# Performance work log

Hardware: AMD Instinct MI355X
Metric: run time of the kernel (lower is better)

The kernel has to match this reference:

```python
import jax, jax.numpy as jnp
import numpy as np

N = 100000   # nodes
E = 1600000  # edges (avg degree 16)
D = 64       # feature dim
H = 256      # MLP hidden
EPS = 0.0    # init_eps, learn_eps=False


def setup_inputs() -> dict:
    key = jax.random.key(0)
    k = jax.random.split(key, 5)
    feat = jax.random.normal(k[0], (N, D), dtype=jnp.float32)
    W1 = jax.random.normal(k[1], (D, H), dtype=jnp.float32) / np.sqrt(D)
    b1 = jnp.zeros((H,), dtype=jnp.float32)
    W2 = jax.random.normal(k[2], (H, D), dtype=jnp.float32) / np.sqrt(H)
    b2 = jnp.zeros((D,), dtype=jnp.float32)
    src = jax.random.randint(k[3], (E,), 0, N, dtype=jnp.int32)
    dst = jax.random.randint(k[4], (E,), 0, N, dtype=jnp.int32)
    return {"feat": feat, "W1": W1, "b1": b1, "W2": W2, "b2": b2,
            "src": src, "dst": dst}


def reference(feat, W1, b1, W2, b2, src, dst):
    # message: m_e = feat[src_e]; reduce: sum over edges into dst
    neigh = jax.ops.segment_sum(feat[src], dst, num_segments=N)  # [N, D]
    # eps-scaled self loop (no edge features => feat_dst unpadded)
    rst = (1.0 + EPS) * feat + neigh
    # apply_func: 2-layer MLP with ReLU
    h = jax.nn.relu(rst @ W1 + b1)
    return h @ W2 + b2
```

## Files before the change

kernel.cpp:

```cpp
#include <hip/hip_runtime.h>

#define D 64
#define H 256
#define SRC_MASK ((1u << 23) - 1)

#define NBF 512
#define NPBF 256
#define CAPF 4096
#define PJ 8
#define PROUNDS 2

#define NB2 512
#define NPB2 256
#define CAP2 6144
#define PEPT 16

typedef __bf16 bf16x8 __attribute__((ext_vector_type(8)));
typedef float f32x16 __attribute__((ext_vector_type(16)));
typedef unsigned int uint4v __attribute__((ext_vector_type(4)));

__device__ inline unsigned pack_bf16x2(float a, float b) {
    unsigned short ua = __builtin_bit_cast(unsigned short, (__bf16)a);
    unsigned short ub = __builtin_bit_cast(unsigned short, (__bf16)b);
    return (unsigned)ua | ((unsigned)ub << 16);
}

__device__ inline void lane32_swap(unsigned x, unsigned y, unsigned& o0, unsigned& o1) {
#if __has_builtin(__builtin_amdgcn_permlane32_swap)
    typedef unsigned int uint2v __attribute__((ext_vector_type(2)));
    uint2v r = __builtin_amdgcn_permlane32_swap(x, y, false, false);
    o0 = r.x; o1 = r.y;
#else
    unsigned xs = __shfl_xor((int)x, 32, 64);
    unsigned ys = __shfl_xor((int)y, 32, 64);
    bool hi = (threadIdx.x & 32) != 0;
    o0 = hi ? ys : x;
    o1 = hi ? y : xs;
#endif
}

__device__ inline bf16x8 weight_frag(const float* __restrict__ W1,
                                     const float* __restrict__ W2,
                                     int fid, int lane) {
    int g = lane >> 5, c = lane & 31;
    bf16x8 v;
    if (fid < 32) {
        int ht = fid >> 2, ks = fid & 3;
        const float* col = W1 + (32 * ht + c);
        int k0 = 16 * ks + 8 * g;
#pragma unroll
        for (int j = 0; j < 8; ++j) v[j] = (__bf16)col[(size_t)(k0 + j) * H];
    } else {
        int f = fid - 32;
        int dt = f >> 4, ks = f & 15;
        const float* col = W2 + (32 * dt + c);
        int k0 = 16 * ks + 8 * g;
#pragma unroll
        for (int j = 0; j < 8; ++j) v[j] = (__bf16)col[(size_t)(k0 + j) * D];
    }
    return v;
}

__global__ __launch_bounds__(1024) void fused_front_kernel(
        const float* __restrict__ feat, unsigned short* __restrict__ featb,
        int n8v,
        const float* __restrict__ W1, const float* __restrict__ W2,
        bf16x8* __restrict__ wf,
        const int* __restrict__ src, const int* __restrict__ dst,
        int* __restrict__ cur,
        unsigned* __restrict__ packed, uint2* __restrict__ ovf,
        int E, int npb, int pB, int prepB) {
    int blk = blockIdx.x;
    int tid = threadIdx.x;

    if (blk >= pB + prepB) {
        int i = (blk - pB - prepB) * 1024 + tid;
        if (i < n8v) {
            const float4* f4 = reinterpret_cast<const float4*>(feat);
            float4 a = f4[2 * i];
            float4 b = f4[2 * i + 1];
            uint4v o = { pack_bf16x2(a.x, a.y), pack_bf16x2(a.z, a.w),
                         pack_bf16x2(b.x, b.y), pack_bf16x2(b.z, b.w) };
            reinterpret_cast<uint4v*>(featb)[i] = o;
        }
        return;
    }
    if (blk >= pB) {
        int fid = (blk - pB) * 16 + (tid >> 6);
        int lane = tid & 63;
        if (fid < 64) wf[fid * 64 + lane] = weight_frag(W1, W2, fid, lane);
        return;
    }

    __shared__ int cnt[NBF];
    __shared__ int resv[NBF];
    int base_e = blk * (1024 * PJ * PROUNDS);
    for (int r = 0; r < PROUNDS; ++r) {
        if (tid < NBF) cnt[tid] = 0;
        __syncthreads();
        int e0 = base_e + r * (1024 * PJ);
        unsigned myP[PJ];
        int myB[PJ], myR[PJ];
#pragma unroll
        for (int j = 0; j < PJ; ++j) {
            int e = e0 + j * 1024 + tid;
            if (e < E) {
                int d = dst[e];
                int s = src[e];
                int b = (int)((unsigned)d / (unsigned)npb);
                myB[j] = b;
                myR[j] = atomicAdd(&cnt[b], 1);
                myP[j] = ((unsigned)(d - b * npb) << 23) | (unsigned)s;
            } else {
                myB[j] = -1;
            }
        }
        __syncthreads();
        if (tid < NBF && cnt[tid] > 0)
            resv[tid] = atomicAdd(&cur[tid], cnt[tid]);
        __syncthreads();
#pragma unroll
        for (int j = 0; j < PJ; ++j) {
            if (myB[j] < 0) continue;
            int slot = resv[myB[j]] + myR[j];
            if (slot < CAPF) {
                packed[(size_t)myB[j] * CAPF + slot] = myP[j];
            } else {
                int oi = atomicAdd(&cur[NBF], 1);
                ovf[oi] = make_uint2(((unsigned)myB[j] << 16) | (myP[j] >> 23),
                                     myP[j] & SRC_MASK);
            }
        }
        if (r + 1 < PROUNDS) __syncthreads();
    }
}

__global__ __launch_bounds__(1024, 2) void csr_gather_fixed_kernel(
        const unsigned* __restrict__ packed, const int* __restrict__ cur,
        const uint2* __restrict__ ovf,
        const unsigned short* __restrict__ featb,
        unsigned short* __restrict__ rstb, int n, int npb) {
    __shared__ int hist[NPBF];
    __shared__ int start[NPBF];
    __shared__ int cursor[NPBF];
    __shared__ unsigned raw[CAPF];
    __shared__ int srt[CAPF];

    int b = blockIdx.x;
    int tid = threadIdx.x;
    int node0 = b * npb;

    if (tid < NPBF) hist[tid] = 0;
    __syncthreads();

    int stored = cur[b];
    if (stored > CAPF) stored = CAPF;
    int ovfn = cur[NBF];
    const unsigned* win = packed + (size_t)b * CAPF;

    for (int k = tid; k < stored; k += 1024) {
        unsigned p = win[k];
        raw[k] = p;
        atomicAdd(&hist[p >> 23], 1);
    }
    __syncthreads();

    if (tid < NPBF) start[tid] = hist[tid];
    __syncthreads();
    for (int o = 1; o < NPBF; o <<= 1) {
        int t = (tid < NPBF && tid >= o) ? start[tid - o] : 0;
        __syncthreads();
        if (tid < NPBF) start[tid] += t;
        __syncthreads();
    }
    if (tid < NPBF) {
        int ex = start[tid] - hist[tid];
        start[tid] = ex;
        cursor[tid] = ex;
    }
    __syncthreads();

    for (int k = tid; k < stored; k += 1024) {
        unsigned p = raw[k];
        int pos = atomicAdd(&cursor[p >> 23], 1);
        srt[pos] = (int)(p & SRC_MASK);
    }
    __syncthreads();

    int g = tid & 7;
    const bf16x8* f8 = reinterpret_cast<const bf16x8*>(featb);
    for (int ln = tid >> 3; ln < npb; ln += 128) {
        int node = node0 + ln;
        if (node >= n) break;
        bf16x8 self = f8[node * 8 + g];
        float acc[8];
#pragma unroll
        for (int j = 0; j < 8; ++j) acc[j] = (float)self[j];

        int s0 = start[ln];
        int e1 = s0 + hist[ln];
        int i = s0;
        for (; i + 4 <= e1; i += 4) {
            int u0 = srt[i + 0];
            int u1 = srt[i + 1];
            int u2 = srt[i + 2];
            int u3 = srt[i + 3];
            bf16x8 v0 = f8[u0 * 8 + g];
            bf16x8 v1 = f8[u1 * 8 + g];
            bf16x8 v2 = f8[u2 * 8 + g];
            bf16x8 v3 = f8[u3 * 8 + g];
#pragma unroll
            for (int j = 0; j < 8; ++j)
                acc[j] += ((float)v0[j] + (float)v1[j]) +
                          ((float)v2[j] + (float)v3[j]);
        }
        for (; i < e1; ++i) {
            bf16x8 v = f8[srt[i] * 8 + g];
#pragma unroll
            for (int j = 0; j < 8; ++j) acc[j] += (float)v[j];
        }
        if (ovfn > 0) {
            unsigned key = ((unsigned)b << 16) | (unsigned)ln;
            for (int k = 0; k < ovfn; ++k) {
                uint2 oe = ovf[k];
                if (oe.x == key) {
                    bf16x8 v = f8[oe.y * 8 + g];
#pragma unroll
                    for (int j = 0; j < 8; ++j) acc[j] += (float)v[j];
                }
            }
        }

        uint4v o = { pack_bf16x2(acc[0], acc[1]), pack_bf16x2(acc[2], acc[3]),
                     pack_bf16x2(acc[4], acc[5]), pack_bf16x2(acc[6], acc[7]) };
        reinterpret_cast<uint4v*>(rstb)[node * 8 + g] = o;
    }
}

__global__ void prep_weights_kernel(const float* __restrict__ W1,
                                    const float* __restrict__ W2,
                                    bf16x8* __restrict__ wf,
                                    int* __restrict__ gz) {
    if (blockIdx.x >= 64) {
        for (int i = threadIdx.x; i < 2 * NB2; i += 64) gz[i] = 0;
        return;
    }
    wf[blockIdx.x * 64 + threadIdx.x] =
        weight_frag(W1, W2, blockIdx.x, threadIdx.x);
}

__global__ __launch_bounds__(256) void cvt_hist_kernel(
        const float* __restrict__ feat, unsigned short* __restrict__ featb,
        int n8, const int* __restrict__ dst, int E, int* __restrict__ gcnt,
        int npb, int nb, int cvtB) {
    int tid = threadIdx.x;
    if ((int)blockIdx.x < cvtB) {
        int i = blockIdx.x * 256 + tid;
        if (i < n8) {
            const float4* f4 = reinterpret_cast<const float4*>(feat);
            float4 a = f4[2 * i];
            float4 b = f4[2 * i + 1];
            uint4v o = { pack_bf16x2(a.x, a.y), pack_bf16x2(a.z, a.w),
                         pack_bf16x2(b.x, b.y), pack_bf16x2(b.z, b.w) };
            reinterpret_cast<uint4v*>(featb)[i] = o;
        }
    } else {
        __shared__ int c[NB2];
        for (int i = tid; i < NB2; i += 256) c[i] = 0;
        __syncthreads();
        int hb = gridDim.x - cvtB;
        for (int e = (blockIdx.x - cvtB) * 256 + tid; e < E; e += hb * 256)
            atomicAdd(&c[(unsigned)dst[e] / (unsigned)npb], 1);
        __syncthreads();
        for (int i = tid; i < nb; i += 256)
            if (c[i] > 0) atomicAdd(&gcnt[i], c[i]);
    }
}

__global__ __launch_bounds__(1024) void partition2_kernel(
        const int* __restrict__ src, const int* __restrict__ dst,
        const int* __restrict__ gcnt, int* __restrict__ cur2,
        unsigned* __restrict__ packed, int E, int npb, int nb) {
    __shared__ int sg[NB2];
    __shared__ int cnt[NB2];
    __shared__ int base_s[NB2];
    int tid = threadIdx.x;
    if (tid < NB2) {
        sg[tid] = (tid < nb) ? gcnt[tid] : 0;
        cnt[tid] = 0;
    }
    __syncthreads();
    for (int o = 1; o < NB2; o <<= 1) {
        int t = (tid < NB2 && tid >= o) ? sg[tid - o] : 0;
        __syncthreads();
        if (tid < NB2) sg[tid] += t;
        __syncthreads();
    }
    int e0 = blockIdx.x * (1024 * PEPT);
    unsigned myP[PEPT];
    int myB[PEPT], myR[PEPT];
#pragma unroll
    for (int j = 0; j < PEPT; ++j) {
        int e = e0 + j * 1024 + tid;
        if (e < E) {
            int d = dst[e];
            int s = src[e];
            int b = (unsigned)d / (unsigned)npb;
            myB[j] = b;
            myR[j] = atomicAdd(&cnt[b], 1);
            myP[j] = ((unsigned)(d - b * npb) << 23) | (unsigned)s;
        } else {
            myB[j] = -1;
        }
    }
    __syncthreads();
    if (tid < nb && cnt[tid] > 0)
        base_s[tid] = (sg[tid] - gcnt[tid]) + atomicAdd(&cur2[tid], cnt[tid]);
    __syncthreads();
#pragma unroll
    for (int j = 0; j < PEPT; ++j) {
        if (myB[j] >= 0) packed[base_s[myB[j]] + myR[j]] = myP[j];
    }
}

__global__ __launch_bounds__(1024, 2) void csr_gather2_kernel(
        const unsigned* __restrict__ packed, const int* __restrict__ gcnt,
        const unsigned short* __restrict__ featb,
        int* __restrict__ csr_g, unsigned short* __restrict__ rstb,
        int n, int npb, int nb) {
    __shared__ int sg[NB2];
    __shared__ int hist[NPB2];
    __shared__ int start[NPB2];
    __shared__ int cursor[NPB2];
    __shared__ unsigned raw[CAP2];
    __shared__ int srt[CAP2];

    int b = blockIdx.x;
    int tid = threadIdx.x;
    int node0 = b * npb;

    if (tid < NB2) sg[tid] = (tid < nb) ? gcnt[tid] : 0;
    if (tid < NPB2) hist[tid] = 0;
    __syncthreads();
    for (int o = 1; o < NB2; o <<= 1) {
        int t = (tid < NB2 && tid >= o) ? sg[tid - o] : 0;
        __syncthreads();
        if (tid < NB2) sg[tid] += t;
        __syncthreads();
    }
    int ie = sg[b];
    int ib = (b > 0) ? sg[b - 1] : 0;
    bool useG = (ie - ib) > CAP2;

    for (int k = ib + tid; k < ie; k += 1024) {
        unsigned p = packed[k];
        if (!useG) raw[k - ib] = p;
        atomicAdd(&hist[p >> 23], 1);
    }
    __syncthreads();

    if (tid < NPB2) start[tid] = hist[tid];
    __syncthreads();
    for (int o = 1; o < NPB2; o <<= 1) {
        int t = (tid < NPB2 && tid >= o) ? start[tid - o] : 0;
        __syncthreads();
        if (tid < NPB2) start[tid] += t;
        __syncthreads();
    }
    if (tid < NPB2) {
        int excl = start[tid] - hist[tid];
        start[tid] = excl;
        cursor[tid] = excl;
    }
    __syncthreads();

    int cnt_e = ie - ib;
    if (!useG) {
        for (int k = tid; k < cnt_e; k += 1024) {
            unsigned p = raw[k];
            int pos = atomicAdd(&cursor[p >> 23], 1);
            srt[pos] = (int)(p & SRC_MASK);
        }
    } else {
        for (int k = ib + tid; k < ie; k += 1024) {
            unsigned p = packed[k];
            int pos = atomicAdd(&cursor[p >> 23], 1);
            csr_g[ib + pos] = (int)(p & SRC_MASK);
        }
    }
    __syncthreads();

    int g = tid & 7;
    const bf16x8* f8 = reinterpret_cast<const bf16x8*>(featb);
    for (int ln = tid >> 3; ln < npb; ln += 128) {
        int node = node0 + ln;
        if (node >= n) break;
        bf16x8 self = f8[node * 8 + g];
        float acc[8];
#pragma unroll
        for (int j = 0; j < 8; ++j) acc[j] = (float)self[j];

        int s0 = start[ln];
        int e1 = s0 + hist[ln];
        const int* lst = useG ? (csr_g + ib) : srt;
        int i = s0;
        for (; i + 4 <= e1; i += 4) {
            int u0 = lst[i + 0];
            int u1 = lst[i + 1];
            int u2 = lst[i + 2];
            int u3 = lst[i + 3];
            bf16x8 v0 = f8[u0 * 8 + g];
            bf16x8 v1 = f8[u1 * 8 + g];
            bf16x8 v2 = f8[u2 * 8 + g];
            bf16x8 v3 = f8[u3 * 8 + g];
#pragma unroll
            for (int j = 0; j < 8; ++j)
                acc[j] += ((float)v0[j] + (float)v1[j]) +
                          ((float)v2[j] + (float)v3[j]);
        }
        for (; i < e1; ++i) {
            bf16x8 v = f8[lst[i] * 8 + g];
#pragma unroll
            for (int j = 0; j < 8; ++j) acc[j] += (float)v[j];
        }

        uint4v o = { pack_bf16x2(acc[0], acc[1]), pack_bf16x2(acc[2], acc[3]),
                     pack_bf16x2(acc[4], acc[5]), pack_bf16x2(acc[6], acc[7]) };
        reinterpret_cast<uint4v*>(rstb)[node * 8 + g] = o;
    }
}

template <bool BF16>
__global__ __launch_bounds__(512, 4) void mlp_mfma_kernel(
        const void* __restrict__ rstv, const bf16x8* __restrict__ wf,
        const float* __restrict__ b1, const float* __restrict__ b2,
        float* __restrict__ out, int n, int ntiles) {
    __shared__ bf16x8 swf[64 * 64];
    __shared__ float sb1[H];
    __shared__ float sb2[D];

    for (int i = threadIdx.x; i < 64 * 64; i += 512) swf[i] = wf[i];
    if (threadIdx.x < H) sb1[threadIdx.x] = b1[threadIdx.x];
    if (threadIdx.x < D) sb2[threadIdx.x] = b2[threadIdx.x];
    __syncthreads();

    int lane = threadIdx.x & 63;
    int wid  = threadIdx.x >> 6;
    int g = lane >> 5, c = lane & 31;

    int tile = blockIdx.x * 8 + wid;
    if (tile >= ntiles) return;
    int node = tile * 32 + c;
    bool valid = node < n;
    int nodeC = valid ? node : (n - 1);

    bf16x8 bfr[4];
    if constexpr (BF16) {
        const bf16x8* rb = reinterpret_cast<const bf16x8*>(rstv) +
                           (size_t)nodeC * 8 + g;
#pragma unroll
        for (int ks = 0; ks < 4; ++ks) bfr[ks] = rb[2 * ks];
    } else {
        const float* rrow = reinterpret_cast<const float*>(rstv) +
                            (size_t)nodeC * D + 8 * g;
#pragma unroll
        for (int ks = 0; ks < 4; ++ks) {
            float4 lo = *reinterpret_cast<const float4*>(rrow + 16 * ks);
            float4 hi = *reinterpret_cast<const float4*>(rrow + 16 * ks + 4);
            bf16x8 v;
            v[0] = (__bf16)lo.x; v[1] = (__bf16)lo.y; v[2] = (__bf16)lo.z; v[3] = (__bf16)lo.w;
            v[4] = (__bf16)hi.x; v[5] = (__bf16)hi.y; v[6] = (__bf16)hi.z; v[7] = (__bf16)hi.w;
            bfr[ks] = v;
        }
    }

    f32x16 acc2_0 = {};
    f32x16 acc2_1 = {};

#pragma unroll
    for (int ht = 0; ht < 8; ++ht) {
        f32x16 a1 = {};
#pragma unroll
        for (int ks = 0; ks < 4; ++ks)
            a1 = __builtin_amdgcn_mfma_f32_32x32x16_bf16(
                     swf[(ht * 4 + ks) * 64 + lane], bfr[ks], a1, 0, 0, 0);

        float hv[16];
#pragma unroll
        for (int q = 0; q < 4; ++q) {
            float4 bq = *reinterpret_cast<const float4*>(&sb1[32 * ht + 8 * q + 4 * g]);
            hv[4 * q + 0] = fmaxf(a1[4 * q + 0] + bq.x, 0.0f);
            hv[4 * q + 1] = fmaxf(a1[4 * q + 1] + bq.y, 0.0f);
            hv[4 * q + 2] = fmaxf(a1[4 * q + 2] + bq.z, 0.0f);
            hv[4 * q + 3] = fmaxf(a1[4 * q + 3] + bq.w, 0.0f);
        }

#pragma unroll
        for (int half = 0; half < 2; ++half) {
            const float* hs = hv + 8 * half;
            unsigned plo0 = pack_bf16x2(hs[0], hs[1]);
            unsigned plo1 = pack_bf16x2(hs[2], hs[3]);
            unsigned phi0 = pack_bf16x2(hs[4], hs[5]);
            unsigned phi1 = pack_bf16x2(hs[6], hs[7]);
            unsigned f0, f2, f1, f3;
            lane32_swap(plo0, phi0, f0, f2);
            lane32_swap(plo1, phi1, f1, f3);
            uint4v fr = { f0, f1, f2, f3 };
            bf16x8 b2f = __builtin_bit_cast(bf16x8, fr);
            int ks2 = 2 * ht + half;
            acc2_0 = __builtin_amdgcn_mfma_f32_32x32x16_bf16(
                         swf[(32 + 0 * 16 + ks2) * 64 + lane], b2f, acc2_0, 0, 0, 0);
            acc2_1 = __builtin_amdgcn_mfma_f32_32x32x16_bf16(
                         swf[(32 + 1 * 16 + ks2) * 64 + lane], b2f, acc2_1, 0, 0, 0);
        }
    }

    if (!valid) return;
    float* orow = out + (size_t)node * D;
#pragma unroll
    for (int dt = 0; dt < 2; ++dt) {
        const f32x16& a = dt ? acc2_1 : acc2_0;
#pragma unroll
        for (int q = 0; q < 4; ++q) {
            int d0 = 32 * dt + 8 * q + 4 * g;
            float4 bq = *reinterpret_cast<const float4*>(&sb2[d0]);
            float4 v;
            v.x = a[4 * q + 0] + bq.x;
            v.y = a[4 * q + 1] + bq.y;
            v.z = a[4 * q + 2] + bq.z;
            v.w = a[4 * q + 3] + bq.w;
            *reinterpret_cast<float4*>(orow + d0) = v;
        }
    }
}

__global__ void copy_feat_kernel(const float* __restrict__ feat,
                                 float* __restrict__ rst, int n4) {
    int i = blockIdx.x * blockDim.x + threadIdx.x;
    if (i < n4) {
        reinterpret_cast<float4*>(rst)[i] =
            reinterpret_cast<const float4*>(feat)[i];
    }
}

__global__ void scatter_add_kernel(const float* __restrict__ feat,
                                   const int* __restrict__ src,
                                   const int* __restrict__ dst,
                                   float* rst, int E) {
    int gid = blockIdx.x * blockDim.x + threadIdx.x;
    int e = gid >> 4;
    if (e >= E) return;
    int d4 = (gid & 15) << 2;
    int s = src[e];
    int t = dst[e];
    float4 v = *reinterpret_cast<const float4*>(&feat[s * D + d4]);
    float* p = &rst[t * D + d4];
    atomicAdd(p + 0, v.x);
    atomicAdd(p + 1, v.y);
    atomicAdd(p + 2, v.z);
    atomicAdd(p + 3, v.w);
}

__global__ __launch_bounds__(512) void mlp_valu_kernel(
        const float* rst,
        const float* __restrict__ W1, const float* __restrict__ b1,
        const float* __restrict__ W2, const float* __restrict__ b2,
        float* out, int n) {
    __shared__ float sW1t[H * D];
    __shared__ float sW2 [H * D];
    __shared__ float sb1[H];
    __shared__ float sb2[D];

    for (int i = threadIdx.x; i < D * H; i += 512) {
        int d = i >> 8;
        int j = i & (H - 1);
        sW1t[j * D + d] = W1[i];
        sW2[i] = W2[i];
    }
    if (threadIdx.x < H) sb1[threadIdx.x] = b1[threadIdx.x];
    if (threadIdx.x < D) sb2[threadIdx.x] = b2[threadIdx.x];
    __syncthreads();

    int node = blockIdx.x * 512 + threadIdx.x;
    if (node >= n) return;

    float x[D];
    const float4* xr = reinterpret_cast<const float4*>(&rst[node * D]);
#pragma unroll
    for (int d4 = 0; d4 < D / 4; ++d4) {
        float4 v = xr[d4];
        x[d4 * 4 + 0] = v.x; x[d4 * 4 + 1] = v.y;
        x[d4 * 4 + 2] = v.z; x[d4 * 4 + 3] = v.w;
    }
    float acc[D];
#pragma unroll
    for (int d = 0; d < D; ++d) acc[d] = sb2[d];
    for (int j = 0; j < H; ++j) {
        float h = sb1[j];
        const float4* w1 = reinterpret_cast<const float4*>(&sW1t[j * D]);
#pragma unroll
        for (int d4 = 0; d4 < D / 4; ++d4) {
            float4 w = w1[d4];
            h += x[d4 * 4 + 0] * w.x + x[d4 * 4 + 1] * w.y +
                 x[d4 * 4 + 2] * w.z + x[d4 * 4 + 3] * w.w;
        }
        h = fmaxf(h, 0.0f);
        const float4* w2 = reinterpret_cast<const float4*>(&sW2[j * D]);
#pragma unroll
        for (int d4 = 0; d4 < D / 4; ++d4) {
            float4 w = w2[d4];
            acc[d4 * 4 + 0] += h * w.x; acc[d4 * 4 + 1] += h * w.y;
            acc[d4 * 4 + 2] += h * w.z; acc[d4 * 4 + 3] += h * w.w;
        }
    }
    float4* op = reinterpret_cast<float4*>(&out[node * D]);
#pragma unroll
    for (int d4 = 0; d4 < D / 4; ++d4) {
        float4 v;
        v.x = acc[d4 * 4 + 0]; v.y = acc[d4 * 4 + 1];
        v.z = acc[d4 * 4 + 2]; v.w = acc[d4 * 4 + 3];
        op[d4] = v;
    }
}

extern "C" void kernel_launch(void* const* d_in, const int* in_sizes, int n_in,
                              void* d_out, int out_size, void* d_ws, size_t ws_size,
                              hipStream_t stream) {
    const float* feat = (const float*)d_in[0];
    const float* W1   = (const float*)d_in[1];
    const float* b1   = (const float*)d_in[2];
    const float* W2   = (const float*)d_in[3];
    const float* b2   = (const float*)d_in[4];
    const int*   src  = (const int*)d_in[5];
    const int*   dst  = (const int*)d_in[6];
    float* buf = (float*)d_out;

    int n = in_sizes[0] / D;
    int E = in_sizes[5];
    char* ws = (char*)d_ws;

    int npbF = (n + NBF - 1) / NBF;
    int nbF  = (n + npbF - 1) / npbF;
    size_t o1 = 0;
    auto a1 = [&](size_t bytes) { size_t c = o1; o1 = (o1 + bytes + 255) & ~(size_t)255; return c; };
    size_t t1_wf     = a1(64 * 64 * sizeof(bf16x8));
    size_t t1_ctrl   = a1((NBF + 1) * sizeof(int));
    size_t t1_packed = a1((size_t)NBF * CAPF * sizeof(unsigned));
    size_t t1_ovf    = a1((size_t)E * sizeof(uint2));
    size_t t1_featb  = a1((size_t)n * D * 2);
    size_t t1_rstb   = a1((size_t)n * D * 2);
    size_t need1 = o1;
    bool tier1 = (npbF <= NPBF) && (ws_size >= need1);

    if (tier1) {
        bf16x8*   wf     = (bf16x8*)(ws + t1_wf);
        int*      ctrl   = (int*)(ws + t1_ctrl);
        unsigned* packed = (unsigned*)(ws + t1_packed);
        uint2*    ovf    = (uint2*)(ws + t1_ovf);
        unsigned short* featb = (unsigned short*)(ws + t1_featb);
        unsigned short* rstb  = (unsigned short*)(ws + t1_rstb);

        hipMemsetAsync(ctrl, 0, (NBF + 1) * sizeof(int), stream);

        int n8v  = n * D / 8;
        int cvtB = (n8v + 1023) / 1024;
        int pB   = (E + 1024 * PJ * PROUNDS - 1) / (1024 * PJ * PROUNDS);
        int prepB = 4;
        fused_front_kernel<<<pB + prepB + cvtB, 1024, 0, stream>>>(
            feat, featb, n8v, W1, W2, wf, src, dst, ctrl, packed, ovf,
            E, npbF, pB, prepB);

        csr_gather_fixed_kernel<<<nbF, 1024, 0, stream>>>(
            packed, ctrl, ovf, featb, rstb, n, npbF);

        int ntiles = (n + 31) / 32;
        mlp_mfma_kernel<true><<<(ntiles + 7) / 8, 512, 0, stream>>>(
            rstb, wf, b1, b2, buf, n, ntiles);
        return;
    }

    int npb2 = (n + NB2 - 1) / NB2;
    int nb2  = (n + npb2 - 1) / npb2;
    size_t o2 = 0;
    auto a2 = [&](size_t bytes) { size_t c = o2; o2 = (o2 + bytes + 255) & ~(size_t)255; return c; };
    size_t t2_wf     = a2(64 * 64 * sizeof(bf16x8));
    size_t t2_gcnt   = a2(2 * NB2 * sizeof(int));
    size_t t2_packed = a2((size_t)E * sizeof(unsigned));
    size_t t2_csrg   = a2((size_t)E * sizeof(int));
    size_t t2_featb  = a2((size_t)n * D * 2);
    size_t t2_rstb   = a2((size_t)n * D * 2);
    size_t need2 = o2;
    bool haveWf = ws_size >= 64 * 64 * sizeof(bf16x8);
    bool tier2  = (npb2 <= NPB2) && (n < (1 << 23)) && (ws_size >= need2);

    if (tier2) {
        bf16x8*   wf     = (bf16x8*)(ws + t2_wf);
        int*      gcnt   = (int*)(ws + t2_gcnt);
        int*      cur2   = gcnt + NB2;
        unsigned* packed = (unsigned*)(ws + t2_packed);
        int*      csr_g  = (int*)(ws + t2_csrg);
        unsigned short* featb = (unsigned short*)(ws + t2_featb);
        unsigned short* rstb  = (unsigned short*)(ws + t2_rstb);

        prep_weights_kernel<<<65, 64, 0, stream>>>(W1, W2, wf, gcnt);

        int n8   = n * D / 8;
        int cvtB = (n8 + 255) / 256;
        cvt_hist_kernel<<<cvtB + 784, 256, 0, stream>>>(
            feat, featb, n8, dst, E, gcnt, npb2, nb2, cvtB);

        int pB2 = (E + 1024 * PEPT - 1) / (1024 * PEPT);
        partition2_kernel<<<pB2, 1024, 0, stream>>>(
            src, dst, gcnt, cur2, packed, E, npb2, nb2);

        csr_gather2_kernel<<<nb2, 1024, 0, stream>>>(
            packed, gcnt, featb, csr_g, rstb, n, npb2, nb2);

        int ntiles = (n + 31) / 32;
        mlp_mfma_kernel<true><<<(ntiles + 7) / 8, 512, 0, stream>>>(
            rstb, wf, b1, b2, buf, n, ntiles);
        return;
    }

    if (haveWf) {
        bf16x8* wf = (bf16x8*)ws;
        prep_weights_kernel<<<64, 64, 0, stream>>>(W1, W2, wf, (int*)ws);
        int n4 = n * D / 4;
        copy_feat_kernel<<<(n4 + 255) / 256, 256, 0, stream>>>(feat, buf, n4);
        int threads = E * 16;
        scatter_add_kernel<<<(threads + 255) / 256, 256, 0, stream>>>(
            feat, src, dst, buf, E);
        int ntiles = (n + 31) / 32;
        mlp_mfma_kernel<false><<<(ntiles + 7) / 8, 512, 0, stream>>>(
            buf, wf, b1, b2, buf, n, ntiles);
    } else {
        int n4 = n * D / 4;
        copy_feat_kernel<<<(n4 + 255) / 256, 256, 0, stream>>>(feat, buf, n4);
        int threads = E * 16;
        scatter_add_kernel<<<(threads + 255) / 256, 256, 0, stream>>>(
            feat, src, dst, buf, E);
        mlp_valu_kernel<<<(n + 511) / 512, 512, 0, stream>>>(
            buf, W1, b1, W2, b2, buf, n);
    }
}
```

Before: 79.87 us.

## Rework gather thread mapping and amortize MLP weight staging over multiple tiles

The CSR gather now assigns four threads per node, each doing four passes over 8-byte slices. It replaces the earlier eight threads per node with 16-byte loads, converts bf16 with bit shifts, and uses nontemporal loads and stores. The MLP kernel now processes four 32-node tiles per wave, so each block stages the weight fragments into shared memory once for four times as many nodes, and the grid is shrunk to match. The trade is fewer blocks and less parallelism in both kernels in exchange for less redundant weight loading and different memory access granularity.

After: 152.8 us. +91.3%, slower.

```diff
diff --git a/kernel.cpp b/kernel.cpp
--- a/kernel.cpp
+++ b/kernel.cpp
@@ -9,6 +9,7 @@
 #define CAPF 4096
 #define PJ 8
 #define PROUNDS 2
+#define TPW 4
 
 #define NB2 512
 #define NPB2 256
@@ -18,11 +19,18 @@
 typedef __bf16 bf16x8 __attribute__((ext_vector_type(8)));
 typedef float f32x16 __attribute__((ext_vector_type(16)));
 typedef unsigned int uint4v __attribute__((ext_vector_type(4)));
+typedef unsigned long long u64;
 
 __device__ inline unsigned pack_bf16x2(float a, float b) {
     unsigned short ua = __builtin_bit_cast(unsigned short, (__bf16)a);
     unsigned short ub = __builtin_bit_cast(unsigned short, (__bf16)b);
     return (unsigned)ua | ((unsigned)ub << 16);
+}
+__device__ inline float bf_lo(unsigned u) {
+    return __builtin_bit_cast(float, u << 16);
+}
+__device__ inline float bf_hi(unsigned u) {
+    return __builtin_bit_cast(float, u & 0xffff0000u);
 }
 
 __device__ inline void lane32_swap(unsigned x, unsigned y, unsigned& o0, unsigned& o1) {
@@ -159,7 +167,7 @@
     const unsigned* win = packed + (size_t)b * CAPF;
 
     for (int k = tid; k < stored; k += 1024) {
-        unsigned p = win[k];
+        unsigned p = __builtin_nontemporal_load(win + k);
         raw[k] = p;
         atomicAdd(&hist[p >> 23], 1);
     }
@@ -187,53 +195,66 @@
     }
     __syncthreads();
 
-    int g = tid & 7;
-    const bf16x8* f8 = reinterpret_cast<const bf16x8*>(featb);
-    for (int ln = tid >> 3; ln < npb; ln += 128) {
-        int node = node0 + ln;
-        if (node >= n) break;
-        bf16x8 self = f8[node * 8 + g];
-        float acc[8];
-#pragma unroll
-        for (int j = 0; j < 8; ++j) acc[j] = (float)self[j];
-
-        int s0 = start[ln];
-        int e1 = s0 + hist[ln];
+    int q  = tid & 3;
+    int ln = tid >> 2;
+    int node = node0 + ln;
+    bool act = (ln < npb) && (node < n);
+    int s0 = 0, e1 = 0;
+    if (act) { s0 = start[ln]; e1 = s0 + hist[ln]; }
+
+    const u64* f8 = reinterpret_cast<const u64*>(featb);
+    u64* r8 = reinterpret_cast<u64*>(rstb);
+
+#pragma unroll 1
+    for (int p = 0; p < 4; ++p) {
+        if (!act) continue;
+        int o = (p << 2) | q;
+        size_t nbase = (size_t)node * 16 + o;
+        u64 sv = f8[nbase];
+        float a0 = bf_lo((unsigned)sv),        a1 = bf_hi((unsigned)sv);
+        float a2 = bf_lo((unsigned)(sv >> 32)), a3 = bf_hi((unsigned)(sv >> 32));
+
         int i = s0;
         for (; i + 4 <= e1; i += 4) {
             int u0 = srt[i + 0];
             int u1 = srt[i + 1];
             int u2 = srt[i + 2];
             int u3 = srt[i + 3];
-            bf16x8 v0 = f8[u0 * 8 + g];
-            bf16x8 v1 = f8[u1 * 8 + g];
-            bf16x8 v2 = f8[u2 * 8 + g];
-            bf16x8 v3 = f8[u3 * 8 + g];
-#pragma unroll
-            for (int j = 0; j < 8; ++j)
-                acc[j] += ((float)v0[j] + (float)v1[j]) +
-                          ((float)v2[j] + (float)v3[j]);
+            u64 v0 = f8[(size_t)u0 * 16 + o];
+            u64 v1 = f8[(size_t)u1 * 16 + o];
+            u64 v2 = f8[(size_t)u2 * 16 + o];
+            u64 v3 = f8[(size_t)u3 * 16 + o];
+            a0 += (bf_lo((unsigned)v0) + bf_lo((unsigned)v1)) +
+                  (bf_lo((unsigned)v2) + bf_lo((unsigned)v3));
+            a1 += (bf_hi((unsigned)v0) + bf_hi((unsigned)v1)) +
+                  (bf_hi((unsigned)v2) + bf_hi((unsigned)v3));
+            a2 += (bf_lo((unsigned)(v0 >> 32)) + bf_lo((unsigned)(v1 >> 32))) +
+                  (bf_lo((unsigned)(v2 >> 32)) + bf_lo((unsigned)(v3 >> 32)));
+            a3 += (bf_hi((unsigned)(v0 >> 32)) + bf_hi((unsigned)(v1 >> 32))) +
+                  (bf_hi((unsigned)(v2 >> 32)) + bf_hi((unsigned)(v3 >> 32)));
         }
         for (; i < e1; ++i) {
-            bf16x8 v = f8[srt[i] * 8 + g];
-#pragma unroll
-            for (int j = 0; j < 8; ++j) acc[j] += (float)v[j];
+            u64 v = f8[(size_t)srt[i] * 16 + o];
+            a0 += bf_lo((unsigned)v);
+            a1 += bf_hi((unsigned)v);
+            a2 += bf_lo((unsigned)(v >> 32));
+            a3 += bf_hi((unsigned)(v >> 32));
         }
         if (ovfn > 0) {
             unsigned key = ((unsigned)b << 16) | (unsigned)ln;
             for (int k = 0; k < ovfn; ++k) {
                 uint2 oe = ovf[k];
                 if (oe.x == key) {
-                    bf16x8 v = f8[oe.y * 8 + g];
-#pragma unroll
-                    for (int j = 0; j < 8; ++j) acc[j] += (float)v[j];
+                    u64 v = f8[(size_t)oe.y * 16 + o];
+                    a0 += bf_lo((unsigned)v);
+                    a1 += bf_hi((unsigned)v);
+                    a2 += bf_lo((unsigned)(v >> 32));
+                    a3 += bf_hi((unsigned)(v >> 32));
                 }
             }
         }
-
-        uint4v o = { pack_bf16x2(acc[0], acc[1]), pack_bf16x2(acc[2], acc[3]),
-                     pack_bf16x2(acc[4], acc[5]), pack_bf16x2(acc[6], acc[7]) };
-        reinterpret_cast<uint4v*>(rstb)[node * 8 + g] = o;
+        u64 w = (u64)pack_bf16x2(a0, a1) | ((u64)pack_bf16x2(a2, a3) << 32);
+        __builtin_nontemporal_store(w, r8 + nbase);
     }
 }
 
@@ -448,88 +469,90 @@
     int wid  = threadIdx.x >> 6;
     int g = lane >> 5, c = lane & 31;
 
-    int tile = blockIdx.x * 8 + wid;
-    if (tile >= ntiles) return;
-    int node = tile * 32 + c;
-    bool valid = node < n;
-    int nodeC = valid ? node : (n - 1);
-
-    bf16x8 bfr[4];
-    if constexpr (BF16) {
-        const bf16x8* rb = reinterpret_cast<const bf16x8*>(rstv) +
-                           (size_t)nodeC * 8 + g;
-#pragma unroll
-        for (int ks = 0; ks < 4; ++ks) bfr[ks] = rb[2 * ks];
-    } else {
-        const float* rrow = reinterpret_cast<const float*>(rstv) +
-                            (size_t)nodeC * D + 8 * g;
-#pragma unroll
-        for (int ks = 0; ks < 4; ++ks) {
-            float4 lo = *reinterpret_cast<const float4*>(rrow + 16 * ks);
-            float4 hi = *reinterpret_cast<const float4*>(rrow + 16 * ks + 4);
-            bf16x8 v;
-            v[0] = (__bf16)lo.x; v[1] = (__bf16)lo.y; v[2] = (__bf16)lo.z; v[3] = (__bf16)lo.w;
-            v[4] = (__bf16)hi.x; v[5] = (__bf16)hi.y; v[6] = (__bf16)hi.z; v[7] = (__bf16)hi.w;
-            bfr[ks] = v;
-        }
-    }
-
-    f32x16 acc2_0 = {};
-    f32x16 acc2_1 = {};
-
-#pragma unroll
-    for (int ht = 0; ht < 8; ++ht) {
-        f32x16 a1 = {};
-#pragma unroll
-        for (int ks = 0; ks < 4; ++ks)
-            a1 = __builtin_amdgcn_mfma_f32_32x32x16_bf16(
-                     swf[(ht * 4 + ks) * 64 + lane], bfr[ks], a1, 0, 0, 0);
-
-        float hv[16];
-#pragma unroll
-        for (int q = 0; q < 4; ++q) {
-            float4 bq = *reinterpret_cast<const float4*>(&sb1[32 * ht + 8 * q + 4 * g]);
-            hv[4 * q + 0] = fmaxf(a1[4 * q + 0] + bq.x, 0.0f);
-            hv[4 * q + 1] = fmaxf(a1[4 * q + 1] + bq.y, 0.0f);
-            hv[4 * q + 2] = fmaxf(a1[4 * q + 2] + bq.z, 0.0f);
-            hv[4 * q + 3] = fmaxf(a1[4 * q + 3] + bq.w, 0.0f);
-        }
-
-#pragma unroll
-        for (int half = 0; half < 2; ++half) {
-            const float* hs = hv + 8 * half;
-            unsigned plo0 = pack_bf16x2(hs[0], hs[1]);
-            unsigned plo1 = pack_bf16x2(hs[2], hs[3]);
-            unsigned phi0 = pack_bf16x2(hs[4], hs[5]);
-            unsigned phi1 = pack_bf16x2(hs[6], hs[7]);
-            unsigned f0, f2, f1, f3;
-            lane32_swap(plo0, phi0, f0, f2);
-            lane32_swap(plo1, phi1, f1, f3);
-            uint4v fr = { f0, f1, f2, f3 };
-            bf16x8 b2f = __builtin_bit_cast(bf16x8, fr);
-            int ks2 = 2 * ht + half;
-            acc2_0 = __builtin_amdgcn_mfma_f32_32x32x16_bf16(
-                         swf[(32 + 0 * 16 + ks2) * 64 + lane], b2f, acc2_0, 0, 0, 0);
-            acc2_1 = __builtin_amdgcn_mfma_f32_32x32x16_bf16(
-                         swf[(32 + 1 * 16 + ks2) * 64 + lane], b2f, acc2_1, 0, 0, 0);
-        }
-    }
-
-    if (!valid) return;
-    float* orow = out + (size_t)node * D;
-#pragma unroll
-    for (int dt = 0; dt < 2; ++dt) {
-        const f32x16& a = dt ? acc2_1 : acc2_0;
-#pragma unroll
-        for (int q = 0; q < 4; ++q) {
-            int d0 = 32 * dt + 8 * q + 4 * g;
-            float4 bq = *reinterpret_cast<const float4*>(&sb2[d0]);
-            float4 v;
-            v.x = a[4 * q + 0] + bq.x;
-            v.y = a[4 * q + 1] + bq.y;
-            v.z = a[4 * q + 2] + bq.z;
-            v.w = a[4 * q + 3] + bq.w;
-            *reinterpret_cast<float4*>(orow + d0) = v;
+    for (int t = 0; t < TPW; ++t) {
+        int tile = (blockIdx.x * 8 + wid) * TPW + t;
+        if (tile >= ntiles) break;
+        int node = tile * 32 + c;
+        bool valid = node < n;
+        int nodeC = valid ? node : (n - 1);
+
+        bf16x8 bfr[4];
+        if constexpr (BF16) {
+            const bf16x8* rb = reinterpret_cast<const bf16x8*>(rstv) +
+                               (size_t)nodeC * 8 + g;
+#pragma unroll
+            for (int ks = 0; ks < 4; ++ks) bfr[ks] = rb[2 * ks];
+        } else {
+            const float* rrow = reinterpret_cast<const float*>(rstv) +
+                                (size_t)nodeC * D + 8 * g;
+#pragma unroll
+            for (int ks = 0; ks < 4; ++ks) {
+                float4 lo = *reinterpret_cast<const float4*>(rrow + 16 * ks);
+                float4 hi = *reinterpret_cast<const float4*>(rrow + 16 * ks + 4);
+                bf16x8 v;
+                v[0] = (__bf16)lo.x; v[1] = (__bf16)lo.y; v[2] = (__bf16)lo.z; v[3] = (__bf16)lo.w;
+                v[4] = (__bf16)hi.x; v[5] = (__bf16)hi.y; v[6] = (__bf16)hi.z; v[7] = (__bf16)hi.w;
+                bfr[ks] = v;
+            }
+        }
+
+        f32x16 acc2_0 = {};
+        f32x16 acc2_1 = {};
+
+#pragma unroll
+        for (int ht = 0; ht < 8; ++ht) {
+            f32x16 a1 = {};
+#pragma unroll
+            for (int ks = 0; ks < 4; ++ks)
+                a1 = __builtin_amdgcn_mfma_f32_32x32x16_bf16(
+                         swf[(ht * 4 + ks) * 64 + lane], bfr[ks], a1, 0, 0, 0);
+
+            float hv[16];
+#pragma unroll
+            for (int q = 0; q < 4; ++q) {
+                float4 bq = *reinterpret_cast<const float4*>(&sb1[32 * ht + 8 * q + 4 * g]);
+                hv[4 * q + 0] = fmaxf(a1[4 * q + 0] + bq.x, 0.0f);
+                hv[4 * q + 1] = fmaxf(a1[4 * q + 1] + bq.y, 0.0f);
+                hv[4 * q + 2] = fmaxf(a1[4 * q + 2] + bq.z, 0.0f);
+                hv[4 * q + 3] = fmaxf(a1[4 * q + 3] + bq.w, 0.0f);
+            }
+
+#pragma unroll
+            for (int half = 0; half < 2; ++half) {
+                const float* hs = hv + 8 * half;
+                unsigned plo0 = pack_bf16x2(hs[0], hs[1]);
+                unsigned plo1 = pack_bf16x2(hs[2], hs[3]);
+                unsigned phi0 = pack_bf16x2(hs[4], hs[5]);
+                unsigned phi1 = pack_bf16x2(hs[6], hs[7]);
+                unsigned f0, f2, f1, f3;
+                lane32_swap(plo0, phi0, f0, f2);
+                lane32_swap(plo1, phi1, f1, f3);
+                uint4v fr = { f0, f1, f2, f3 };
+                bf16x8 b2f = __builtin_bit_cast(bf16x8, fr);
+                int ks2 = 2 * ht + half;
+                acc2_0 = __builtin_amdgcn_mfma_f32_32x32x16_bf16(
+                             swf[(32 + 0 * 16 + ks2) * 64 + lane], b2f, acc2_0, 0, 0, 0);
+                acc2_1 = __builtin_amdgcn_mfma_f32_32x32x16_bf16(
+                             swf[(32 + 1 * 16 + ks2) * 64 + lane], b2f, acc2_1, 0, 0, 0);
+            }
+        }
+
+        if (!valid) continue;
+        float* orow = out + (size_t)node * D;
+#pragma unroll
+        for (int dt = 0; dt < 2; ++dt) {
+            const f32x16& a = dt ? acc2_1 : acc2_0;
+#pragma unroll
+            for (int q = 0; q < 4; ++q) {
+                int d0 = 32 * dt + 8 * q + 4 * g;
+                float4 bq = *reinterpret_cast<const float4*>(&sb2[d0]);
+                float4 v;
+                v.x = a[4 * q + 0] + bq.x;
+                v.y = a[4 * q + 1] + bq.y;
+                v.z = a[4 * q + 2] + bq.z;
+                v.w = a[4 * q + 3] + bq.w;
+                *reinterpret_cast<float4*>(orow + d0) = v;
+            }
         }
     }
 }
@@ -674,7 +697,8 @@
             packed, ctrl, ovf, featb, rstb, n, npbF);
 
         int ntiles = (n + 31) / 32;
-        mlp_mfma_kernel<true><<<(ntiles + 7) / 8, 512, 0, stream>>>(
+        int mblocks = (ntiles + 8 * TPW - 1) / (8 * TPW);
+        mlp_mfma_kernel<true><<<mblocks, 512, 0, stream>>>(
             rstb, wf, b1, b2, buf, n, ntiles);
         return;
     }
@@ -717,7 +741,8 @@
             packed, gcnt, featb, csr_g, rstb, n, npb2, nb2);
 
         int ntiles = (n + 31) / 32;
-        mlp_mfma_kernel<true><<<(ntiles + 7) / 8, 512, 0, stream>>>(
+        int mblocks = (ntiles + 8 * TPW - 1) / (8 * TPW);
+        mlp_mfma_kernel<true><<<mblocks, 512, 0, stream>>>(
             rstb, wf, b1, b2, buf, n, ntiles);
         return;
     }
@@ -731,7 +756,8 @@
         scatter_add_kernel<<<(threads + 255) / 256, 256, 0, stream>>>(
             feat, src, dst, buf, E);
         int ntiles = (n + 31) / 32;
-        mlp_mfma_kernel<false><<<(ntiles + 7) / 8, 512, 0, stream>>>(
+        int mblocks = (ntiles + 8 * TPW - 1) / (8 * TPW);
+        mlp_mfma_kernel<false><<<mblocks, 512, 0, stream>>>(
             buf, wf, b1, b2, buf, n, ntiles);
     } else {
         int n4 = n * D / 4;
```
